# Performance work log

Measured on AMD Instinct MI355X. Metric: run time of the kernel, lower is better.

The kernel has to match this reference:

```python
import jax, jax.numpy as jnp
import numpy as np
import math

FEAT_DIM = 128
N_BANK = 1000000
K_NEG = 4096
BATCH = 256
T = 0.5
MOMENTUM = 0.5
EPS = 1e-7


def setup_inputs() -> dict:
    key = jax.random.key(0)
    k1, k2, k3, k4, k5, k6 = jax.random.split(key, 6)
    stdv = 1.0 / math.sqrt(FEAT_DIM / 3)
    memory_l = jax.random.uniform(k1, (N_BANK, FEAT_DIM), minval=-stdv, maxval=stdv, dtype=jnp.float32)
    memory_ab = jax.random.uniform(k2, (N_BANK, FEAT_DIM), minval=-stdv, maxval=stdv, dtype=jnp.float32)
    l = jax.random.normal(k3, (BATCH, FEAT_DIM), dtype=jnp.float32)
    ab = jax.random.normal(k4, (BATCH, FEAT_DIM), dtype=jnp.float32)
    y = jax.random.randint(k5, (BATCH,), 0, N_BANK, dtype=jnp.int32)
    idx = jax.random.randint(k6, (BATCH, K_NEG + 1), 0, N_BANK, dtype=jnp.int32)
    idx = idx.at[:, 0].set(y)  # positive sample in slot 0, as in torch forward
    return {"l": l, "ab": ab, "memory_l": memory_l, "memory_ab": memory_ab, "y": y, "idx": idx}


def _l2_normalize(x):
    # matches torch: x / (sqrt(sum(x^2)) + eps)
    return x / (jnp.sqrt(jnp.sum(x * x, axis=1, keepdims=True)) + EPS)


def _momentum_update(memory, y, x_norm):
    # gather rows, momentum mix, renormalize, scatter back
    pos = memory[y] * MOMENTUM + x_norm * (1.0 - MOMENTUM)          # [B, D]
    norm = jnp.sqrt(jnp.sum(pos * pos, axis=1, keepdims=True))
    return memory.at[y].set(pos / norm)


def reference(l, ab, memory_l, memory_ab, y, idx):
    outputSize = memory_l.shape[0]
    ln = _l2_normalize(l)
    abn = _l2_normalize(ab)

    # gather negatives+positive from the AB bank, score against l features
    w_ab = jax.lax.stop_gradient(memory_ab[idx])                     # [B, K+1, D]
    P_l = jnp.exp(jnp.einsum('bkd,bd->bk', w_ab, ln) / T)[..., None]  # [B, K+1, 1]
    Z_l = jnp.mean(P_l) * outputSize
    out_l = P_l / Z_l

    w_l = jax.lax.stop_gradient(memory_l[idx])                       # [B, K+1, D]
    P_ab = jnp.exp(jnp.einsum('bkd,bd->bk', w_l, abn) / T)[..., None]
    Z_ab = jnp.mean(P_ab) * outputSize
    out_ab = P_ab / Z_ab

    # momentum scatter update of the memory banks (no_grad in torch)
    new_memory_l = jax.lax.stop_gradient(_momentum_update(memory_l, y, ln))
    new_memory_ab = jax.lax.stop_gradient(_momentum_update(memory_ab, y, abn))

    return out_l, out_ab, new_memory_l, new_memory_ab
```

## Files before the change

kernel.cpp:

```cpp
#include <hip/hip_runtime.h>
#include <math.h>

#define FEAT   128
#define NBANK  1000000
#define KP1    4097
#define BATCH  256
#define INV_T  2.0f
#define EPS_N  1e-7f

constexpr size_t TOTP   = (size_t)BATCH * KP1;
constexpr size_t O_OUTL = 0;
constexpr size_t O_OUTA = TOTP;
constexpr size_t O_MEML = 2 * TOTP;
constexpr size_t O_MEMA = O_MEML + (size_t)NBANK * FEAT;

constexpr int KCHUNK = 64;
constexpr int NCHUNK = (KP1 + KCHUNK - 1) / KCHUNK;
constexpr int NPART  = BATCH * NCHUNK;

constexpr int SCOREB = BATCH * NCHUNK;
constexpr int COPYB  = SCOREB / 8;
constexpr int TOTB   = SCOREB + COPYB;

constexpr size_t WS_LN    = 0;
constexpr size_t WS_ABN   = WS_LN + (size_t)BATCH * FEAT;
constexpr size_t WS_PARTL = WS_ABN + (size_t)BATCH * FEAT;
constexpr size_t WS_PARTA = WS_PARTL + NPART;
constexpr size_t WS_INVZ  = WS_PARTA + NPART;

typedef float vfloat4 __attribute__((ext_vector_type(4)));

__device__ __forceinline__ vfloat4 nt_load4(const vfloat4* p) {
    return __builtin_nontemporal_load(p);
}
__device__ __forceinline__ void nt_store4(vfloat4* p, vfloat4 v) {
    __builtin_nontemporal_store(v, p);
}

__global__ void norm_kernel(const float* __restrict__ l,
                            const float* __restrict__ ab,
                            float* __restrict__ ws) {
    int b    = blockIdx.x;
    int lane = threadIdx.x;
    const float* src;
    float*       dst;
    if (b < BATCH) { src = l  + (size_t)b * FEAT;            dst = ws + WS_LN  + (size_t)b * FEAT; }
    else           { src = ab + (size_t)(b - BATCH) * FEAT;  dst = ws + WS_ABN + (size_t)(b - BATCH) * FEAT; }
    float2 v = *(const float2*)(src + 2 * lane);
    float  ss = v.x * v.x + v.y * v.y;
    #pragma unroll
    for (int m = 1; m < 64; m <<= 1) ss += __shfl_xor(ss, m, 64);
    float inv = 1.0f / (sqrtf(ss) + EPS_N);
    ((float2*)dst)[lane] = make_float2(v.x * inv, v.y * inv);
}

__global__ __launch_bounds__(256) void fused_kernel(
        const float* __restrict__ mem_l, const float* __restrict__ mem_ab,
        const int*   __restrict__ idx,
        const float* __restrict__ ws_in,
        float* __restrict__ out,
        float* __restrict__ part_l, float* __restrict__ part_ab) {
    int bid = blockIdx.x;
    if ((bid % 9) == 8) {
        int cid = bid / 9;
        size_t n4 = (size_t)NBANK * FEAT / 4;
        size_t stride = (size_t)COPYB * 256;
        const vfloat4* a  = (const vfloat4*)mem_l;
        const vfloat4* bb = (const vfloat4*)mem_ab;
        vfloat4* ol = (vfloat4*)(out + O_MEML);
        vfloat4* oa = (vfloat4*)(out + O_MEMA);
        for (size_t i = (size_t)cid * 256 + threadIdx.x; i < n4; i += stride) {
            nt_store4(ol + i, nt_load4(a + i));
            nt_store4(oa + i, nt_load4(bb + i));
        }
        return;
    }
    int sid   = (bid / 9) * 8 + (bid % 9);
    int b     = sid % BATCH;
    int chunk = sid / BATCH;
    int wave  = threadIdx.x >> 6;
    int lane  = threadIdx.x & 63;

    float2 lv = *(const float2*)(ws_in + WS_LN  + (size_t)b * FEAT + 2 * lane);
    float2 av = *(const float2*)(ws_in + WS_ABN + (size_t)b * FEAT + 2 * lane);

    float sum_l = 0.f, sum_ab = 0.f;
    int k0 = chunk * KCHUNK + wave * (KCHUNK / 4);
    #pragma unroll 4
    for (int i = 0; i < KCHUNK / 4; ++i) {
        int k = k0 + i;
        if (k >= KP1) break;
        int row = idx[(size_t)b * KP1 + k];
        float2 wa = ((const float2*)(mem_ab + (size_t)row * FEAT))[lane];
        float2 wl = ((const float2*)(mem_l  + (size_t)row * FEAT))[lane];
        float dl  = wa.x * lv.x + wa.y * lv.y;
        float dab = wl.x * av.x + wl.y * av.y;
        #pragma unroll
        for (int m = 1; m < 64; m <<= 1) {
            dl  += __shfl_xor(dl,  m, 64);
            dab += __shfl_xor(dab, m, 64);
        }
        float pl  = expf(dl * INV_T);
        float pab = expf(dab * INV_T);
        if (lane == 0) {
            out[O_OUTL + (size_t)b * KP1 + k] = pl;
            out[O_OUTA + (size_t)b * KP1 + k] = pab;
        }
        sum_l += pl; sum_ab += pab;
    }
    __shared__ float s[8];
    if (lane == 0) { s[wave] = sum_l; s[4 + wave] = sum_ab; }
    __syncthreads();
    if (threadIdx.x == 0) {
        part_l[(size_t)b * NCHUNK + chunk]  = s[0] + s[1] + s[2] + s[3];
        part_ab[(size_t)b * NCHUNK + chunk] = s[4] + s[5] + s[6] + s[7];
    }
}

__global__ void zreduce_kernel(const float* __restrict__ part_l,
                               const float* __restrict__ part_ab,
                               float* __restrict__ invz) {
    __shared__ float sl[256], sa[256];
    float a = 0.f, b = 0.f;
    for (int i = threadIdx.x; i < NPART; i += 256) { a += part_l[i]; b += part_ab[i]; }
    sl[threadIdx.x] = a; sa[threadIdx.x] = b;
    __syncthreads();
    for (int s = 128; s > 0; s >>= 1) {
        if (threadIdx.x < (unsigned)s) {
            sl[threadIdx.x] += sl[threadIdx.x + s];
            sa[threadIdx.x] += sa[threadIdx.x + s];
        }
        __syncthreads();
    }
    if (threadIdx.x == 0) {
        float count = (float)TOTP;
        invz[0] = count / (sl[0] * (float)NBANK);
        invz[1] = count / (sa[0] * (float)NBANK);
    }
}

__global__ void scale_kernel(float* __restrict__ out, const float* __restrict__ invz) {
    float zl = invz[0], za = invz[1];
    size_t stride = (size_t)gridDim.x * blockDim.x;
    for (size_t i = (size_t)blockIdx.x * blockDim.x + threadIdx.x; i < TOTP; i += stride) {
        out[O_OUTL + i] *= zl;
        out[O_OUTA + i] *= za;
    }
}

__global__ void update_kernel(const float* __restrict__ mem_l,
                              const float* __restrict__ mem_ab,
                              const int*   __restrict__ y,
                              const float* __restrict__ ws,
                              float* __restrict__ out) {
    int b    = blockIdx.x;
    int lane = threadIdx.x;
    int row  = y[b];
    for (int j = b + 1; j < BATCH; ++j)
        if (y[j] == row) return;
    {
        float2 m = ((const float2*)(mem_l + (size_t)row * FEAT))[lane];
        float2 x = ((const float2*)(ws + WS_LN + (size_t)b * FEAT))[lane];
        float2 p = make_float2(m.x * 0.5f + x.x * 0.5f, m.y * 0.5f + x.y * 0.5f);
        float ss = p.x * p.x + p.y * p.y;
        #pragma unroll
        for (int mk = 1; mk < 64; mk <<= 1) ss += __shfl_xor(ss, mk, 64);
        float nrm = sqrtf(ss);
        ((float2*)(out + O_MEML + (size_t)row * FEAT))[lane] =
            make_float2(p.x / nrm, p.y / nrm);
    }
    {
        float2 m = ((const float2*)(mem_ab + (size_t)row * FEAT))[lane];
        float2 x = ((const float2*)(ws + WS_ABN + (size_t)b * FEAT))[lane];
        float2 p = make_float2(m.x * 0.5f + x.x * 0.5f, m.y * 0.5f + x.y * 0.5f);
        float ss = p.x * p.x + p.y * p.y;
        #pragma unroll
        for (int mk = 1; mk < 64; mk <<= 1) ss += __shfl_xor(ss, mk, 64);
        float nrm = sqrtf(ss);
        ((float2*)(out + O_MEMA + (size_t)row * FEAT))[lane] =
            make_float2(p.x / nrm, p.y / nrm);
    }
}

extern "C" void kernel_launch(void* const* d_in, const int* in_sizes, int n_in,
                              void* d_out, int out_size, void* d_ws, size_t ws_size,
                              hipStream_t stream) {
    const float* l      = (const float*)d_in[0];
    const float* ab     = (const float*)d_in[1];
    const float* mem_l  = (const float*)d_in[2];
    const float* mem_ab = (const float*)d_in[3];
    const int*   y      = (const int*)d_in[4];
    const int*   idx    = (const int*)d_in[5];
    float* out = (float*)d_out;
    float* ws  = (float*)d_ws;

    norm_kernel<<<dim3(2 * BATCH), dim3(64), 0, stream>>>(l, ab, ws);
    fused_kernel<<<dim3(TOTB), dim3(256), 0, stream>>>(
        mem_l, mem_ab, idx, ws, out, ws + WS_PARTL, ws + WS_PARTA);
    zreduce_kernel<<<dim3(1), dim3(256), 0, stream>>>(ws + WS_PARTL, ws + WS_PARTA, ws + WS_INVZ);
    scale_kernel<<<dim3(1024), dim3(256), 0, stream>>>(out, ws + WS_INVZ);
    update_kernel<<<dim3(BATCH), dim3(64), 0, stream>>>(mem_l, mem_ab, y, ws, out);
}
```

Baseline: 598.0 us.

## Interleave bank copy into every score block and score four rows per wave

```diff
diff --git a/kernel.cpp b/kernel.cpp
--- a/kernel.cpp
+++ b/kernel.cpp
@@ -17,10 +17,10 @@
 constexpr int KCHUNK = 64;
 constexpr int NCHUNK = (KP1 + KCHUNK - 1) / KCHUNK;
 constexpr int NPART  = BATCH * NCHUNK;
-
 constexpr int SCOREB = BATCH * NCHUNK;
-constexpr int COPYB  = SCOREB / 8;
-constexpr int TOTB   = SCOREB + COPYB;
+
+constexpr size_t N4      = (size_t)NBANK * FEAT / 4;
+constexpr size_t CSTRIDE = (size_t)SCOREB * 256;
 
 constexpr size_t WS_LN    = 0;
 constexpr size_t WS_ABN   = WS_LN + (size_t)BATCH * FEAT;
@@ -30,11 +30,11 @@
 
 typedef float vfloat4 __attribute__((ext_vector_type(4)));
 
-__device__ __forceinline__ vfloat4 nt_load4(const vfloat4* p) {
-    return __builtin_nontemporal_load(p);
-}
 __device__ __forceinline__ void nt_store4(vfloat4* p, vfloat4 v) {
     __builtin_nontemporal_store(v, p);
+}
+__device__ __forceinline__ float dot4(vfloat4 a, vfloat4 b) {
+    return a.x * b.x + a.y * b.y + a.z * b.z + a.w * b.w;
 }
 
 __global__ void norm_kernel(const float* __restrict__ l,
@@ -60,53 +60,65 @@
         const float* __restrict__ ws_in,
         float* __restrict__ out,
         float* __restrict__ part_l, float* __restrict__ part_ab) {
-    int bid = blockIdx.x;
-    if ((bid % 9) == 8) {
-        int cid = bid / 9;
-        size_t n4 = (size_t)NBANK * FEAT / 4;
-        size_t stride = (size_t)COPYB * 256;
-        const vfloat4* a  = (const vfloat4*)mem_l;
-        const vfloat4* bb = (const vfloat4*)mem_ab;
-        vfloat4* ol = (vfloat4*)(out + O_MEML);
-        vfloat4* oa = (vfloat4*)(out + O_MEMA);
-        for (size_t i = (size_t)cid * 256 + threadIdx.x; i < n4; i += stride) {
-            nt_store4(ol + i, nt_load4(a + i));
-            nt_store4(oa + i, nt_load4(bb + i));
-        }
-        return;
-    }
-    int sid   = (bid / 9) * 8 + (bid % 9);
-    int b     = sid % BATCH;
-    int chunk = sid / BATCH;
-    int wave  = threadIdx.x >> 6;
-    int lane  = threadIdx.x & 63;
-
-    float2 lv = *(const float2*)(ws_in + WS_LN  + (size_t)b * FEAT + 2 * lane);
-    float2 av = *(const float2*)(ws_in + WS_ABN + (size_t)b * FEAT + 2 * lane);
+    int sid    = blockIdx.x;
+    int b      = sid % BATCH;
+    int chunk  = sid / BATCH;
+    int wave   = threadIdx.x >> 6;
+    int lane   = threadIdx.x & 63;
+    int lane16 = lane & 15;
+    int g      = lane >> 4;
+
+    const vfloat4* lnp = (const vfloat4*)(ws_in + WS_LN  + (size_t)b * FEAT);
+    const vfloat4* abp = (const vfloat4*)(ws_in + WS_ABN + (size_t)b * FEAT);
+    vfloat4 lv0 = lnp[lane16 * 2], lv1 = lnp[lane16 * 2 + 1];
+    vfloat4 av0 = abp[lane16 * 2], av1 = abp[lane16 * 2 + 1];
+
+    const vfloat4* ca = (const vfloat4*)mem_l;
+    const vfloat4* cb = (const vfloat4*)mem_ab;
+    vfloat4* ol = (vfloat4*)(out + O_MEML);
+    vfloat4* oa = (vfloat4*)(out + O_MEMA);
+    size_t cbase = (size_t)sid * 256 + threadIdx.x;
+
+    const int* idx_b = idx + (size_t)b * KP1;
+    int kw = chunk * KCHUNK + wave * 16;
 
     float sum_l = 0.f, sum_ab = 0.f;
-    int k0 = chunk * KCHUNK + wave * (KCHUNK / 4);
-    #pragma unroll 4
-    for (int i = 0; i < KCHUNK / 4; ++i) {
-        int k = k0 + i;
-        if (k >= KP1) break;
-        int row = idx[(size_t)b * KP1 + k];
-        float2 wa = ((const float2*)(mem_ab + (size_t)row * FEAT))[lane];
-        float2 wl = ((const float2*)(mem_l  + (size_t)row * FEAT))[lane];
-        float dl  = wa.x * lv.x + wa.y * lv.y;
-        float dab = wl.x * av.x + wl.y * av.y;
-        #pragma unroll
-        for (int m = 1; m < 64; m <<= 1) {
+    #pragma unroll
+    for (int t = 0; t < 4; ++t) {
+        #pragma unroll
+        for (int j = 0; j < 2; ++j) {
+            size_t ci = cbase + (size_t)(2 * t + j) * CSTRIDE;
+            if (ci < N4) {
+                nt_store4(ol + ci, ca[ci]);
+                nt_store4(oa + ci, cb[ci]);
+            }
+        }
+        int k = kw + t * 4 + g;
+        bool valid = k < KP1;
+        int row = valid ? idx_b[k] : 0;
+        const vfloat4* pa = (const vfloat4*)(mem_ab + (size_t)row * FEAT) + lane16 * 2;
+        const vfloat4* pw = (const vfloat4*)(mem_l  + (size_t)row * FEAT) + lane16 * 2;
+        vfloat4 wa0 = pa[0], wa1 = pa[1];
+        vfloat4 wl0 = pw[0], wl1 = pw[1];
+        float dl  = dot4(wa0, lv0) + dot4(wa1, lv1);
+        float dab = dot4(wl0, av0) + dot4(wl1, av1);
+        #pragma unroll
+        for (int m = 1; m < 16; m <<= 1) {
             dl  += __shfl_xor(dl,  m, 64);
             dab += __shfl_xor(dab, m, 64);
         }
-        float pl  = expf(dl * INV_T);
-        float pab = expf(dab * INV_T);
-        if (lane == 0) {
+        float pl  = valid ? __expf(dl  * INV_T) : 0.f;
+        float pab = valid ? __expf(dab * INV_T) : 0.f;
+        if (lane16 == 0 && valid) {
             out[O_OUTL + (size_t)b * KP1 + k] = pl;
             out[O_OUTA + (size_t)b * KP1 + k] = pab;
         }
         sum_l += pl; sum_ab += pab;
+    }
+    #pragma unroll
+    for (int m = 16; m < 64; m <<= 1) {
+        sum_l  += __shfl_xor(sum_l,  m, 64);
+        sum_ab += __shfl_xor(sum_ab, m, 64);
     }
     __shared__ float s[8];
     if (lane == 0) { s[wave] = sum_l; s[4 + wave] = sum_ab; }
@@ -195,7 +207,7 @@
     float* ws  = (float*)d_ws;
 
     norm_kernel<<<dim3(2 * BATCH), dim3(64), 0, stream>>>(l, ab, ws);
-    fused_kernel<<<dim3(TOTB), dim3(256), 0, stream>>>(
+    fused_kernel<<<dim3(SCOREB), dim3(256), 0, stream>>>(
         mem_l, mem_ab, idx, ws, out, ws + WS_PARTL, ws + WS_PARTA);
     zreduce_kernel<<<dim3(1), dim3(256), 0, stream>>>(ws + WS_PARTL, ws + WS_PARTA, ws + WS_INVZ);
     scale_kernel<<<dim3(1024), dim3(256), 0, stream>>>(out, ws + WS_INVZ);
```

Measured after the change: 583.2 us. 1.03x faster.
